# Optimization experiments

Measured on AMD Instinct MI355X. Metric: run time of the kernel, lower is better.

## Reference

```python
import jax, jax.numpy as jnp
import numpy as np

K = 5  # kernel_size


def _unfold(x, k):
    """Torch F.unfold equivalent: [B,C,H,W] -> [B,C,k*k,H,W].
    Patch index is row-major over the kxk window (dy*k+dx), matching
    F.unfold's channel-major / window-row-major layout after view(B,C,k*k,H,W)."""
    p = k // 2
    B, C, H, W = x.shape
    xp = jnp.pad(x, ((0, 0), (0, 0), (p, p), (p, p)))
    patches = [xp[:, :, dy:dy + H, dx:dx + W] for dy in range(k) for dx in range(k)]
    return jnp.stack(patches, axis=2)


def _conv2d(x, w, b, pad):
    y = jax.lax.conv_general_dilated(
        x, w, window_strides=(1, 1), padding=[(pad, pad), (pad, pad)],
        dimension_numbers=("NCHW", "OIHW", "NCHW"))
    return y + b[None, :, None, None]


def setup_inputs() -> dict:
    key = jax.random.key(0)
    k0, k1, k2 = jax.random.split(key, 3)
    B, H, W = 2, 1024, 1024
    flow = jax.random.normal(k0, (B, 2, H, W), jnp.float32)
    # kernel_gen params: Conv2d(3,32,3,pad=1) -> ReLU -> Conv2d(32,50,1)
    w1 = jax.random.normal(k1, (32, 3, 3, 3), jnp.float32) * 0.1
    b1 = jnp.zeros((32,), jnp.float32)
    w2 = jax.random.normal(k2, (K * K * 2, 32, 1, 1), jnp.float32) * 0.1
    b2 = jnp.zeros((K * K * 2,), jnp.float32)
    return {"flow": flow, "w1": w1, "b1": b1, "w2": w2, "b2": b2}


def reference(flow, w1, b1, w2, b2):
    B, _, H, W = flow.shape
    patches = _unfold(flow, K)                       # [B,2,25,H,W]
    # torch .var(dim=2) defaults to unbiased (ddof=1)
    var = jnp.var(patches, axis=2, ddof=1)           # [B,2,H,W]
    consistency = jnp.exp(-jnp.sqrt(jnp.sum(var * var, axis=1, keepdims=True)))  # [B,1,H,W]
    guidance = jnp.concatenate([flow, consistency], axis=1)  # [B,3,H,W]
    h = jax.nn.relu(_conv2d(guidance, w1, b1, pad=1))        # [B,32,H,W]
    kernels = _conv2d(h, w2, b2, pad=0).reshape(B, 2, K * K, H, W)
    refined = jnp.sum(kernels * patches, axis=2)             # [B,2,H,W]
    return refined
```

## Files before the change

kernel.cpp:

```cpp
#include <hip/hip_runtime.h>
#include <math.h>

#define KSZ 5
#define TSX 16
#define TSY 64
#define HALO 3
#define FWX 22
#define FH  70
#define SCH 66
#define PITCH 23
#define SF_C (FH*PITCH)
#define SC_BASE (2*SF_C)
#define SMF_TOT (SC_BASE + SCH*PITCH)

typedef __attribute__((ext_vector_type(8))) short short8_t;
typedef __attribute__((ext_vector_type(4))) float float4_t;

static __device__ __forceinline__ unsigned short f2bf(float f) {
    union { float f; unsigned int u; } v; v.f = f;
    return (unsigned short)((v.u + 0x7FFFu + ((v.u >> 16) & 1u)) >> 16);
}
static __device__ __forceinline__ unsigned int pk2t(float a, float b) {
    union { float f; unsigned int u; } ua, ub; ua.f = a; ub.f = b;
    return __builtin_amdgcn_perm(ub.u, ua.u, 0x07060302u);
}

static __device__ __forceinline__ void slot_decode(int n, int& c, int& sel, int& idx, bool& valid) {
    int g4c = (n >> 2) & 3;
    c = g4c >> 1; sel = g4c & 1;
    idx = ((n >> 4) << 2) + (n & 3);
    valid = sel ? (idx < 10) : (idx < 15);
}

static __device__ __forceinline__ int kperm(int s) {
    int sg = s >> 3, sj = s & 7;
    if (sg < 3) return sg*9 + sj;
    if (sj == 1) return 8;
    if (sj == 2) return 17;
    if (sj == 4) return 26;
    return -1;
}

static __device__ __forceinline__ int kperm2(int s) {
    int g = s >> 3, j = s & 7;
    return (j < 4) ? (g*4 + j) : (16 + g*4 + (j - 4));
}

__global__ __launch_bounds__(256)
void pack_kernel(const float* __restrict__ w1, const float* __restrict__ b1,
                 const float* __restrict__ w2, const float* __restrict__ b2,
                 unsigned short* __restrict__ wp, float* __restrict__ bp)
{
    const int tid = threadIdx.x;
    for (int i = tid; i < 6*64*8; i += 256) {
        int f = i >> 9, l = (i >> 3) & 63, j = i & 7;
        int m = l & 15, s = ((l >> 4) << 3) + j;
        float v;
        if (f < 2) {
            int k = kperm(s);
            v = (k >= 0) ? w1[(f*16 + m)*27 + k] : 0.f;
        } else {
            int n = (f - 2)*16 + m;
            int c, sel, idx; bool valid;
            slot_decode(n, c, sel, idx, valid);
            v = valid ? w2[(c*25 + sel*15 + idx)*32 + kperm2(s)] : 0.f;
        }
        wp[i] = f2bf(v);
    }
    for (int i = tid; i < 6*64*4; i += 256) {
        int f = i >> 8, l = (i >> 2) & 63, r = i & 3, g4 = l >> 4;
        float v;
        if (f < 2) v = b1[f*16 + g4*4 + r];
        else {
            int n = (f - 2)*16 + g4*4 + r;
            int c, sel, idx; bool valid;
            slot_decode(n, c, sel, idx, valid);
            v = valid ? b2[c*25 + sel*15 + idx] : 0.f;
        }
        bp[i] = v;
    }
}

__global__ __launch_bounds__(256, 4)
void refine_kernel(const float* __restrict__ flow,
                   const unsigned short* __restrict__ wp,
                   const float* __restrict__ bp,
                   float* __restrict__ out, int H, int W)
{
    __shared__ float smf[SMF_TOT];
    __shared__ __align__(16) float4_t rs[FH*18];

    const int tid = threadIdx.x;
    const int x0 = blockIdx.x * TSX;
    const int y0 = blockIdx.y * TSY;
    const int b  = blockIdx.z;

    const int lane = tid & 63;
    const int wave = tid >> 6;
    const int col  = lane & 15;
    const int g4   = lane >> 4;

    short8_t w1A[2], w2A[4];
    float4_t cb1[2], cb2[4];
    #pragma unroll
    for (int nt = 0; nt < 2; ++nt) {
        w1A[nt] = *(const short8_t*)&wp[(nt*64 + lane)*8];
        cb1[nt] = *(const float4_t*)&bp[(nt*64 + lane)*4];
    }
    #pragma unroll
    for (int nt = 0; nt < 4; ++nt) {
        w2A[nt] = *(const short8_t*)&wp[((2+nt)*64 + lane)*8];
        cb2[nt] = *(const float4_t*)&bp[((2+nt)*64 + lane)*4];
    }

    {
        const float* srcb = flow + (size_t)(b*2) * H * W;
        if (x0 >= HALO && x0 + TSX + HALO <= W && y0 >= HALO && y0 + TSY + HALO <= H) {
            const float* s = srcb + (size_t)(y0 - HALO) * W + (x0 - HALO);
            for (int i = tid; i < 2*FH*FWX; i += 256) {
                int c = 0, r = i;
                if (r >= FH*FWX) { c = 1; r -= FH*FWX; }
                int ly = r / FWX, lx = r - ly*FWX;
                smf[c*SF_C + ly*PITCH + lx] = s[(size_t)c*H*W + ly*W + lx];
            }
        } else {
            for (int i = tid; i < 2*FH*FWX; i += 256) {
                int c = 0, r = i;
                if (r >= FH*FWX) { c = 1; r -= FH*FWX; }
                int ly = r / FWX, lx = r - ly*FWX;
                int gy = y0 - HALO + ly, gx = x0 - HALO + lx;
                float v = 0.f;
                if (gy >= 0 && gy < H && gx >= 0 && gx < W)
                    v = srcb[(size_t)c*H*W + (size_t)gy*W + gx];
                smf[c*SF_C + ly*PITCH + lx] = v;
            }
        }
    }
    __syncthreads();

    for (int i = tid; i < FH*9; i += 256) {
        int y = i / 9, xp = (i - y*9) * 2;
        const float* r0 = &smf[y*PITCH + xp];
        const float* r1 = &smf[SF_C + y*PITCH + xp];
        float a0=r0[0], a1=r0[1], a2=r0[2], a3=r0[3], a4=r0[4], a5=r0[5];
        float c0=r1[0], c1=r1[1], c2=r1[2], c3=r1[3], c4=r1[4], c5=r1[5];
        float sA = ((a0+a1)+(a2+a3))+a4;
        float qA = fmaf(a4,a4, fmaf(a3,a3, fmaf(a2,a2, fmaf(a1,a1, a0*a0))));
        float sB = ((c0+c1)+(c2+c3))+c4;
        float qB = fmaf(c4,c4, fmaf(c3,c3, fmaf(c2,c2, fmaf(c1,c1, c0*c0))));
        float sA1 = sA + a5 - a0;
        float qA1 = fmaf(-a0, a0, fmaf(a5, a5, qA));
        float sB1 = sB + c5 - c0;
        float qB1 = fmaf(-c0, c0, fmaf(c5, c5, qB));
        rs[y*18 + xp]     = (float4_t){sA,  qA,  sB,  qB };
        rs[y*18 + xp + 1] = (float4_t){sA1, qA1, sB1, qB1};
    }
    __syncthreads();

    for (int i = tid; i < (SCH/2)*18; i += 256) {
        int u = i / 18, px = i - u*18;
        int py0 = u*2;
        int gx = x0 - 1 + px;
        int gy0 = y0 - 1 + py0;
        const float4_t* rp = rs + py0*18 + px;
        float4_t r0 = rp[0], r1 = rp[18], r2 = rp[2*18], r3 = rp[3*18],
                 r4 = rp[4*18], r5 = rp[5*18];
        float4_t mid = (r1 + r2) + (r3 + r4);
        float4_t acc0 = mid + r0;
        float4_t acc1 = mid + r5;
        float cons0 = 0.f, cons1 = 0.f;
        bool okx = (gx >= 0) && (gx < W);
        if (okx && gy0 >= 0 && gy0 < H) {
            float v0 = (acc0.y - acc0.x*acc0.x*(1.f/25.f)) * (1.f/24.f);
            float v1 = (acc0.w - acc0.z*acc0.z*(1.f/25.f)) * (1.f/24.f);
            cons0 = __expf(-sqrtf(v0*v0 + v1*v1));
        }
        if (okx && gy0+1 >= 0 && gy0+1 < H) {
            float v0 = (acc1.y - acc1.x*acc1.x*(1.f/25.f)) * (1.f/24.f);
            float v1 = (acc1.w - acc1.z*acc1.z*(1.f/25.f)) * (1.f/24.f);
            cons1 = __expf(-sqrtf(v0*v0 + v1*v1));
        }
        smf[SC_BASE + py0*PITCH + px]       = cons0;
        smf[SC_BASE + (py0+1)*PITCH + px]   = cons1;
    }
    __syncthreads();

    const int sel = g4 & 1, pc = g4 >> 1;
    const int tyA = wave*16, tyB = wave*16 + 8;

    int gA0, gA1, gA2, gA3, gB0, gB1, gB2, gB3;
    {
        int p0 = 0*SF_C + 2*PITCH + (col + 2);
        int p1 = 1*SF_C + 2*PITCH + (col + 2);
        int p2 = SC_BASE + col;
        int q0, q1, q2, q3;
        if (g4 == 0)      { q0 = q1 = q2 = q3 = p0; }
        else if (g4 == 1) { q0 = q1 = q2 = q3 = p1; }
        else if (g4 == 2) { q0 = q1 = q2 = q3 = p2; }
        else { q0 = p0 + 47; q1 = p1 + 46; q2 = p2 + 24; q3 = p0; }
        gA0 = q0 + tyA*((g4==2) ? PITCH : PITCH);
        gA0 = q0 + tyA*PITCH; gA1 = q1 + tyA*PITCH; gA2 = q2 + tyA*PITCH; gA3 = q3 + tyA*PITCH;
        gB0 = q0 + tyB*PITCH; gB1 = q1 + tyB*PITCH; gB2 = q2 + tyB*PITCH; gB3 = q3 + tyB*PITCH;
    }

    const int pbase = pc*SF_C + sel*(3*PITCH) + PITCH + 1 + col;
    int pbA = pbase + tyA*PITCH, pbB = pbase + tyB*PITCH;
    float pvA[15], pvB[15];
    #pragma unroll
    for (int i = 0; i < 15; ++i) pvA[i] = smf[pbA + (i/5)*PITCH + (i%5)];
    #pragma unroll
    for (int i = 0; i < 15; ++i) pvB[i] = smf[pbB + (i/5)*PITCH + (i%5)];

    #pragma unroll
    for (int mt = 0; mt < 8; ++mt) {
        float sA;
        {
            float ga = smf[gA0 + 0],  gb_ = smf[gA0 + 1];
            float gc = smf[gA1 + 2],  gd  = smf[gA1 + 23];
            float ge = smf[gA2 + 24], gf  = smf[gA2 + 25];
            float gg = smf[gA3 + 46], gh  = smf[gA3 + 47];
            union { unsigned int u[4]; short8_t s; } gu;
            gu.u[0] = pk2t(ga, gb_); gu.u[1] = pk2t(gc, gd);
            gu.u[2] = pk2t(ge, gf);  gu.u[3] = pk2t(gg, gh);
            gA0 += PITCH; gA1 += PITCH; gA2 += PITCH; gA3 += PITCH;
            float4_t h0 = __builtin_amdgcn_mfma_f32_16x16x32_bf16(w1A[0], gu.s, cb1[0], 0, 0, 0);
            float4_t h1 = __builtin_amdgcn_mfma_f32_16x16x32_bf16(w1A[1], gu.s, cb1[1], 0, 0, 0);
            union { unsigned int u[4]; short8_t s; } hu;
            hu.u[0] = pk2t(fmaxf(h0[0],0.f), fmaxf(h0[1],0.f));
            hu.u[1] = pk2t(fmaxf(h0[2],0.f), fmaxf(h0[3],0.f));
            hu.u[2] = pk2t(fmaxf(h1[0],0.f), fmaxf(h1[1],0.f));
            hu.u[3] = pk2t(fmaxf(h1[2],0.f), fmaxf(h1[3],0.f));
            float4_t ka[4];
            #pragma unroll
            for (int nt = 0; nt < 4; ++nt)
                ka[nt] = __builtin_amdgcn_mfma_f32_16x16x32_bf16(w2A[nt], hu.s, cb2[nt], 0, 0, 0);
            float s = 0.f;
            #pragma unroll
            for (int i = 0; i < 15; ++i)
                s = fmaf(ka[i >> 2][i & 3], pvA[i], s);
            if (mt < 7) {
                #pragma unroll
                for (int i = 0; i < 10; ++i) pvA[i] = pvA[i + 5];
                pbA += PITCH;
                #pragma unroll
                for (int i = 10; i < 15; ++i) pvA[i] = smf[pbA + (i/5)*PITCH + (i%5)];
            }
            sA = s;
        }
        float sB;
        {
            float ga = smf[gB0 + 0],  gb_ = smf[gB0 + 1];
            float gc = smf[gB1 + 2],  gd  = smf[gB1 + 23];
            float ge = smf[gB2 + 24], gf  = smf[gB2 + 25];
            float gg = smf[gB3 + 46], gh  = smf[gB3 + 47];
            union { unsigned int u[4]; short8_t s; } gu;
            gu.u[0] = pk2t(ga, gb_); gu.u[1] = pk2t(gc, gd);
            gu.u[2] = pk2t(ge, gf);  gu.u[3] = pk2t(gg, gh);
            gB0 += PITCH; gB1 += PITCH; gB2 += PITCH; gB3 += PITCH;
            float4_t h0 = __builtin_amdgcn_mfma_f32_16x16x32_bf16(w1A[0], gu.s, cb1[0], 0, 0, 0);
            float4_t h1 = __builtin_amdgcn_mfma_f32_16x16x32_bf16(w1A[1], gu.s, cb1[1], 0, 0, 0);
            union { unsigned int u[4]; short8_t s; } hu;
            hu.u[0] = pk2t(fmaxf(h0[0],0.f), fmaxf(h0[1],0.f));
            hu.u[1] = pk2t(fmaxf(h0[2],0.f), fmaxf(h0[3],0.f));
            hu.u[2] = pk2t(fmaxf(h1[0],0.f), fmaxf(h1[1],0.f));
            hu.u[3] = pk2t(fmaxf(h1[2],0.f), fmaxf(h1[3],0.f));
            float4_t ka[4];
            #pragma unroll
            for (int nt = 0; nt < 4; ++nt)
                ka[nt] = __builtin_amdgcn_mfma_f32_16x16x32_bf16(w2A[nt], hu.s, cb2[nt], 0, 0, 0);
            float s = 0.f;
            #pragma unroll
            for (int i = 0; i < 15; ++i)
                s = fmaf(ka[i >> 2][i & 3], pvB[i], s);
            if (mt < 7) {
                #pragma unroll
                for (int i = 0; i < 10; ++i) pvB[i] = pvB[i + 5];
                pbB += PITCH;
                #pragma unroll
                for (int i = 10; i < 15; ++i) pvB[i] = smf[pbB + (i/5)*PITCH + (i%5)];
            }
            sB = s;
        }

        sA += __shfl_xor(sA, 16);
        sB += __shfl_xor(sB, 16);

        if (sel == 0) {
            int x = x0 + col;
            size_t base = ((size_t)(b*2 + pc) * H) * W + x;
            out[base + (size_t)(y0 + tyA + mt) * W] = sA;
            out[base + (size_t)(y0 + tyB + mt) * W] = sB;
        }
    }
}

extern "C" void kernel_launch(void* const* d_in, const int* in_sizes, int n_in,
                              void* d_out, int out_size, void* d_ws, size_t ws_size,
                              hipStream_t stream) {
    const float* flow = (const float*)d_in[0];
    const float* w1   = (const float*)d_in[1];
    const float* b1   = (const float*)d_in[2];
    const float* w2   = (const float*)d_in[3];
    const float* b2   = (const float*)d_in[4];
    float* out = (float*)d_out;

    unsigned short* wp = (unsigned short*)d_ws;
    float* bp = (float*)((char*)d_ws + 8192);

    const int H = 1024, W = 1024;
    const int B = in_sizes[0] / (2 * H * W);

    pack_kernel<<<1, 256, 0, stream>>>(w1, b1, w2, b2, wp, bp);
    dim3 grid(W / TSX, H / TSY, B);
    refine_kernel<<<grid, dim3(256), 0, stream>>>(flow, wp, bp, out, H, W);
}
```

Baseline: 112.6 us.

## Pack row sums to bf16, vectorize halo loads, raise occupancy bound

Stores the per-row partial sums and sums of squares as packed bf16 pairs instead of float4, halving that LDS buffer so more blocks fit per CU. Launch bounds go from 4 to 5 blocks per SM. The interior tile load now uses aligned float2 global reads over a 24-wide window, dropping the first column. The bf16 rounding of sums and squared sums can cause catastrophic cancellation in the variance and shift the consistency values, which risks accuracy.

```diff
diff --git a/kernel.cpp b/kernel.cpp
--- a/kernel.cpp
+++ b/kernel.cpp
@@ -15,6 +15,7 @@
 
 typedef __attribute__((ext_vector_type(8))) short short8_t;
 typedef __attribute__((ext_vector_type(4))) float float4_t;
+typedef __attribute__((ext_vector_type(2))) unsigned int uint2_t;
 
 static __device__ __forceinline__ unsigned short f2bf(float f) {
     union { float f; unsigned int u; } v; v.f = f;
@@ -23,6 +24,12 @@
 static __device__ __forceinline__ unsigned int pk2t(float a, float b) {
     union { float f; unsigned int u; } ua, ub; ua.f = a; ub.f = b;
     return __builtin_amdgcn_perm(ub.u, ua.u, 0x07060302u);
+}
+static __device__ __forceinline__ float bflo(unsigned int u) {
+    union { unsigned int u; float f; } v; v.u = u << 16; return v.f;
+}
+static __device__ __forceinline__ float bfhi(unsigned int u) {
+    union { unsigned int u; float f; } v; v.u = u & 0xffff0000u; return v.f;
 }
 
 static __device__ __forceinline__ void slot_decode(int n, int& c, int& sel, int& idx, bool& valid) {
@@ -81,14 +88,14 @@
     }
 }
 
-__global__ __launch_bounds__(256, 4)
+__global__ __launch_bounds__(256, 5)
 void refine_kernel(const float* __restrict__ flow,
                    const unsigned short* __restrict__ wp,
                    const float* __restrict__ bp,
                    float* __restrict__ out, int H, int W)
 {
     __shared__ float smf[SMF_TOT];
-    __shared__ __align__(16) float4_t rs[FH*18];
+    __shared__ __align__(8) uint2_t rs[FH*18];
 
     const int tid = threadIdx.x;
     const int x0 = blockIdx.x * TSX;
@@ -115,13 +122,16 @@
 
     {
         const float* srcb = flow + (size_t)(b*2) * H * W;
-        if (x0 >= HALO && x0 + TSX + HALO <= W && y0 >= HALO && y0 + TSY + HALO <= H) {
-            const float* s = srcb + (size_t)(y0 - HALO) * W + (x0 - HALO);
-            for (int i = tid; i < 2*FH*FWX; i += 256) {
+        if (x0 >= 4 && x0 + TSX + 4 <= W && y0 >= HALO && y0 + TSY + HALO <= H) {
+            const float* s = srcb + (size_t)(y0 - HALO) * W + (x0 - 4);
+            for (int i = tid; i < 2*FH*12; i += 256) {
                 int c = 0, r = i;
-                if (r >= FH*FWX) { c = 1; r -= FH*FWX; }
-                int ly = r / FWX, lx = r - ly*FWX;
-                smf[c*SF_C + ly*PITCH + lx] = s[(size_t)c*H*W + ly*W + lx];
+                if (r >= FH*12) { c = 1; r -= FH*12; }
+                int ly = r / 12, lx2 = r - ly*12;
+                float2 v = *(const float2*)(s + (size_t)c*H*W + (size_t)ly*W + 2*lx2);
+                int dst = c*SF_C + ly*PITCH + 2*lx2 - 1;
+                if (dst >= 0) smf[dst] = v.x;
+                smf[dst + 1] = v.y;
             }
         } else {
             for (int i = tid; i < 2*FH*FWX; i += 256) {
@@ -152,8 +162,8 @@
         float qA1 = fmaf(-a0, a0, fmaf(a5, a5, qA));
         float sB1 = sB + c5 - c0;
         float qB1 = fmaf(-c0, c0, fmaf(c5, c5, qB));
-        rs[y*18 + xp]     = (float4_t){sA,  qA,  sB,  qB };
-        rs[y*18 + xp + 1] = (float4_t){sA1, qA1, sB1, qB1};
+        rs[y*18 + xp]     = (uint2_t){pk2t(sA,  qA ), pk2t(sB,  qB )};
+        rs[y*18 + xp + 1] = (uint2_t){pk2t(sA1, qA1), pk2t(sB1, qB1)};
     }
     __syncthreads();
 
@@ -162,12 +172,16 @@
         int py0 = u*2;
         int gx = x0 - 1 + px;
         int gy0 = y0 - 1 + py0;
-        const float4_t* rp = rs + py0*18 + px;
-        float4_t r0 = rp[0], r1 = rp[18], r2 = rp[2*18], r3 = rp[3*18],
-                 r4 = rp[4*18], r5 = rp[5*18];
-        float4_t mid = (r1 + r2) + (r3 + r4);
-        float4_t acc0 = mid + r0;
-        float4_t acc1 = mid + r5;
+        const uint2_t* rp = rs + py0*18 + px;
+        float4_t f[6];
+        #pragma unroll
+        for (int k = 0; k < 6; ++k) {
+            uint2_t uu = rp[k*18];
+            f[k] = (float4_t){bflo(uu.x), bfhi(uu.x), bflo(uu.y), bfhi(uu.y)};
+        }
+        float4_t mid  = (f[1] + f[2]) + (f[3] + f[4]);
+        float4_t acc0 = mid + f[0];
+        float4_t acc1 = mid + f[5];
         float cons0 = 0.f, cons1 = 0.f;
         bool okx = (gx >= 0) && (gx < W);
         if (okx && gy0 >= 0 && gy0 < H) {
@@ -198,7 +212,6 @@
         else if (g4 == 1) { q0 = q1 = q2 = q3 = p1; }
         else if (g4 == 2) { q0 = q1 = q2 = q3 = p2; }
         else { q0 = p0 + 47; q1 = p1 + 46; q2 = p2 + 24; q3 = p0; }
-        gA0 = q0 + tyA*((g4==2) ? PITCH : PITCH);
         gA0 = q0 + tyA*PITCH; gA1 = q1 + tyA*PITCH; gA2 = q2 + tyA*PITCH; gA3 = q3 + tyA*PITCH;
         gB0 = q0 + tyB*PITCH; gB1 = q1 + tyB*PITCH; gB2 = q2 + tyB*PITCH; gB3 = q3 + tyB*PITCH;
     }
```

Measured after the change: 144.1 us. +28.0%, slower.
